# Kernel tuning notes

Measured on AMD Instinct MI355X. Metric: run time of the kernel, lower is better.

Reference implementation:

```python
import jax, jax.numpy as jnp
import numpy as np

WIN = 12          # max_relative_position
HEAD_DIM = 64     # E, equals num_units of relative-position tables


def _rel_embed(table, length):
    r = jnp.arange(length)
    idx = jnp.clip(r[None, :] - r[:, None], -WIN, WIN) + WIN  # [L, L]
    return table[idx]  # [L, L, E]


def setup_inputs() -> dict:
    key = jax.random.key(0)
    ks = jax.random.split(key, 7)
    B, L, H, E = 4, 1024, 8, HEAD_DIM
    shp = (B, L, H, E)
    xavier = float(np.sqrt(6.0 / (2 * WIN + 1 + E)))
    return {
        "x": jax.random.normal(ks[0], shp, jnp.float32),
        "y": jax.random.normal(ks[1], shp, jnp.float32),
        "v_x": jax.random.normal(ks[2], shp, jnp.float32),
        "v_y": jax.random.normal(ks[3], shp, jnp.float32),
        "rel_k_table": jax.random.uniform(ks[4], (2 * WIN + 1, E), jnp.float32, -xavier, xavier),
        "rel_vx_table": jax.random.uniform(ks[5], (2 * WIN + 1, E), jnp.float32, -xavier, xavier),
        "rel_vy_table": jax.random.uniform(ks[6], (2 * WIN + 1, E), jnp.float32, -xavier, xavier),
        "attn_mask1": jnp.zeros((1,), jnp.bool_),
        "attn_mask2": jnp.zeros((1,), jnp.bool_),
    }


def reference(x, y, v_x, v_y, rel_k_table, rel_vx_table, rel_vy_table, attn_mask1, attn_mask2):
    B, L, H, E = x.shape
    scale = 1.0 / float(np.sqrt(E))

    rel_k = _rel_embed(rel_k_table, L)    # [L, L, E]
    rel_vy = _rel_embed(rel_vy_table, L)  # [L, L, E]
    rel_vx = _rel_embed(rel_vx_table, L)  # [L, L, E]

    # scores1[b,h,l,s] = <x_bl h, y_bs h> + <x_bl h, rel_k[l,s]>
    scores1 = jnp.einsum('blhe,bshe->bhls', x, y) \
            + jnp.einsum('blhe,lse->bhls', x, rel_k)
    scores2 = jnp.swapaxes(scores1, -2, -1)  # pre-softmax transpose

    A1 = jax.nn.softmax(scale * scores1, axis=-1)  # [B,H,L,S]
    A2 = jax.nn.softmax(scale * scores2, axis=-1)

    V_Y = jnp.einsum('bhls,bshd->bhld', A1, v_y) \
        + jnp.einsum('bhls,lsd->bhld', A1, rel_vy)
    V_X = jnp.einsum('bhls,bshd->bhld', A2, v_x) \
        + jnp.einsum('bhls,lsd->bhld', A2, rel_vx)

    # module returns (V_Y^T, None, V_X^T, None); drop the Nones
    return jnp.swapaxes(V_Y, 1, 2), jnp.swapaxes(V_X, 1, 2)
```

## Files before the change

kernel.cpp:

```cpp
#include <hip/hip_runtime.h>
#include <math.h>

#define LQ 1024
#define RS 512
#define PJ 26
#define NP 32
#define ASCALE 0.18033688f

typedef __attribute__((ext_vector_type(4))) float f32x4;
typedef __attribute__((ext_vector_type(8))) short short8x;

__device__ __forceinline__ unsigned pk2(float a, float b) {
  unsigned r;
  asm("v_cvt_pk_bf16_f32 %0, %1, %2" : "=v"(r) : "v"(a), "v"(b));
  return r;
}

__device__ __forceinline__ int swz(int row, int bc) {
  return row * 128 + (bc ^ ((row & 7) << 4));
}
__device__ __forceinline__ int swzVT(int row, int bc) {
  return row * 128 + (bc ^ ((((row >> 3) ^ row) & 7) << 4));
}

__global__ __launch_bounds__(256) void k_relproj(const float* __restrict__ x,
                                                 const float* __restrict__ relk,
                                                 float* __restrict__ P) {
  __shared__ float rk[25][68];
  __shared__ float xs[64][68];
  const int tid = threadIdx.x;
  const int pair = blockIdx.y, l0 = blockIdx.x * 64;
  const int b = pair >> 3, h = pair & 7;
  for (int i = tid; i < 25 * 64; i += 256) rk[i >> 6][i & 63] = relk[i] * ASCALE;
  const int row = tid >> 2, q = tid & 3;
  const float* xr = x + (size_t)b * 524288 + (size_t)(l0 + row) * RS + h * 64 + q * 16;
#pragma unroll
  for (int i = 0; i < 4; ++i) {
    float4 a = *(const float4*)(xr + i * 4);
    xs[row][q * 16 + i * 4 + 0] = a.x; xs[row][q * 16 + i * 4 + 1] = a.y;
    xs[row][q * 16 + i * 4 + 2] = a.z; xs[row][q * 16 + i * 4 + 3] = a.w;
  }
  __syncthreads();
  float* Pr = P + ((size_t)pair * LQ + l0 + row) * PJ;
  for (int j = q; j < 25; j += 4) {
    float acc = 0.f;
#pragma unroll
    for (int e = 0; e < 64; ++e) acc += xs[row][e] * rk[j][e];
    Pr[j] = acc;
  }
}

__global__ __launch_bounds__(256, 2) void k_fused(
    const float* __restrict__ x, const float* __restrict__ y,
    const float* __restrict__ vx, const float* __restrict__ vy,
    const float* __restrict__ relvx, const float* __restrict__ relvy,
    const float* __restrict__ P_g, float* __restrict__ out_g) {
  __shared__ __align__(16) char U[8192];
  __shared__ __align__(16) char Bb[2][8192];
  __shared__ __align__(16) char Vb[2][8192];
  __shared__ float W[64 * PJ];

  const int tid = threadIdx.x;
  const int p = blockIdx.x;
  const int g = p & 63, bx = p >> 6;
  const int pair = g & 31, mode = g >> 5;
  const int b = pair >> 3, h = pair & 7;
  const int l0 = bx * 64;

  const float* Af = mode ? y : x;
  const float* Bl = mode ? x : y;
  const float* Vv = mode ? vx : vy;
  const float* tb = mode ? relvx : relvy;
  float* outp = out_g + (mode ? 2097152 : 0);

  const float* abase = Af + (size_t)b * 524288 + h * 64;
  const float* bbase = Bl + (size_t)b * 524288 + h * 64;
  const float* vbase = Vv + (size_t)b * 524288 + h * 64;
  const float* Pbase = P_g + (size_t)pair * LQ * PJ;
  float* outb = outp + (size_t)b * 524288 + h * 64;

  const int browA = tid >> 2, bqA = tid & 3;
  const int vsb = tid >> 4, vdb = tid & 15;

  {
    const float* s = abase + (size_t)(l0 + browA) * RS + bqA * 16;
#pragma unroll
    for (int hh = 0; hh < 2; ++hh) {
      float4 a = *(const float4*)(s + hh * 8);
      float4 c = *(const float4*)(s + hh * 8 + 4);
      uint4 u;
      u.x = pk2(a.x * ASCALE, a.y * ASCALE); u.y = pk2(a.z * ASCALE, a.w * ASCALE);
      u.z = pk2(c.x * ASCALE, c.y * ASCALE); u.w = pk2(c.z * ASCALE, c.w * ASCALE);
      *(uint4*)(U + swz(browA, bqA * 32 + hh * 16)) = u;
    }
    const float* sb2 = bbase + (size_t)browA * RS + bqA * 16;
#pragma unroll
    for (int hh = 0; hh < 2; ++hh) {
      float4 a = *(const float4*)(sb2 + hh * 8);
      float4 c = *(const float4*)(sb2 + hh * 8 + 4);
      uint4 u;
      u.x = pk2(a.x, a.y); u.y = pk2(a.z, a.w);
      u.z = pk2(c.x, c.y); u.w = pk2(c.z, c.w);
      *(uint4*)(Bb[0] + swz(browA, bqA * 32 + hh * 16)) = u;
    }
    const float* sv = vbase + (size_t)vsb * 4 * RS + vdb * 4;
    float4 r0 = *(const float4*)(sv);
    float4 r1 = *(const float4*)(sv + RS);
    float4 r2 = *(const float4*)(sv + 2 * RS);
    float4 r3 = *(const float4*)(sv + 3 * RS);
    uint2 w2;
    w2.x = pk2(r0.x, r1.x); w2.y = pk2(r2.x, r3.x);
    *(uint2*)(Vb[0] + swzVT(vdb * 4 + 0, vsb * 8)) = w2;
    w2.x = pk2(r0.y, r1.y); w2.y = pk2(r2.y, r3.y);
    *(uint2*)(Vb[0] + swzVT(vdb * 4 + 1, vsb * 8)) = w2;
    w2.x = pk2(r0.z, r1.z); w2.y = pk2(r2.z, r3.z);
    *(uint2*)(Vb[0] + swzVT(vdb * 4 + 2, vsb * 8)) = w2;
    w2.x = pk2(r0.w, r1.w); w2.y = pk2(r2.w, r3.w);
    *(uint2*)(Vb[0] + swzVT(vdb * 4 + 3, vsb * 8)) = w2;
  }
  for (int i = tid; i < 64 * PJ; i += 256) W[i] = 0.f;
  __syncthreads();

  const int lane = tid & 63, wv = tid >> 6;
  const int col16 = lane & 15, rg = lane >> 4;
  char* ea = U + wv * 2048;

  short8x af0 = *(const short8x*)(U + swz(wv * 16 + col16, rg * 16));
  short8x af1 = *(const short8x*)(U + swz(wv * 16 + col16, 64 + rg * 16));

  const int lloc = wv * 16 + col16;
  const float* ProwB = Pbase + (size_t)(l0 + lloc) * PJ;
  float bL = 0.f, bR = 0.f;
  if (mode == 0) { bL = ProwB[0]; bR = ProwB[24]; }

  f32x4 accO[4];
  float wl = 0.f, wr = 0.f;
  const f32x4 z4 = {0.f, 0.f, 0.f, 0.f};
#pragma unroll
  for (int dt = 0; dt < 4; ++dt) accO[dt] = z4;

  for (int t = 0; t < 16; ++t) {
    const int cb = t & 1, nb = cb ^ 1;
    const int rel0 = t * 64 - l0;
    const bool band = (rel0 >= -74 && rel0 <= 74);

    float4 pb[4], pv[4];
    if (t < 15) {
      const float* s = bbase + (size_t)((t + 1) * 64 + browA) * RS + bqA * 16;
#pragma unroll
      for (int i = 0; i < 4; ++i) pb[i] = *(const float4*)(s + i * 4);
      const float* sv2 = vbase + (size_t)((t + 1) * 64 + vsb * 4) * RS + vdb * 4;
#pragma unroll
      for (int k = 0; k < 4; ++k) pv[k] = *(const float4*)(sv2 + (size_t)k * RS);
    }

    float biasf[16];
    if (!band && mode == 1) {
      const bool right = rel0 > 0;
#pragma unroll
      for (int ct = 0; ct < 4; ++ct)
#pragma unroll
        for (int r = 0; r < 4; ++r)
          biasf[ct * 4 + r] =
              Pbase[(size_t)(t * 64 + ct * 16 + rg * 4 + r) * PJ + (right ? 0 : 24)];
    }

    f32x4 accS[4];
    const char* bB = Bb[cb];
#pragma unroll
    for (int ct = 0; ct < 4; ++ct) {
      short8x bf0 = *(const short8x*)(bB + swz(ct * 16 + col16, rg * 16));
      short8x bf1 = *(const short8x*)(bB + swz(ct * 16 + col16, 64 + rg * 16));
      f32x4 tacc = __builtin_amdgcn_mfma_f32_16x16x32_bf16(bf0, af0, z4, 0, 0, 0);
      accS[ct] = __builtin_amdgcn_mfma_f32_16x16x32_bf16(bf1, af1, tacc, 0, 0, 0);
    }

    if (!band) {
      const bool right = rel0 > 0;
      const float b0 = right ? bR : bL;
#pragma unroll
      for (int ct = 0; ct < 4; ++ct) {
        float e0 = __builtin_exp2f(accS[ct][0] + (mode ? biasf[ct * 4 + 0] : b0));
        float e1 = __builtin_exp2f(accS[ct][1] + (mode ? biasf[ct * 4 + 1] : b0));
        float e2 = __builtin_exp2f(accS[ct][2] + (mode ? biasf[ct * 4 + 2] : b0));
        float e3 = __builtin_exp2f(accS[ct][3] + (mode ? biasf[ct * 4 + 3] : b0));
        float s4 = (e0 + e1) + (e2 + e3);
        if (right) wr += s4; else wl += s4;
        uint2 w2; w2.x = pk2(e0, e1); w2.y = pk2(e2, e3);
        *(uint2*)(ea + swz(col16, ct * 32 + rg * 8)) = w2;
      }
    } else {
#pragma unroll
      for (int ct = 0; ct < 4; ++ct) {
        float e[4];
#pragma unroll
        for (int r = 0; r < 4; ++r) {
          const int sl = ct * 16 + rg * 4 + r;
          const int d = rel0 + sl - lloc;
          const int j = (d < -12 ? -12 : (d > 12 ? 12 : d)) + 12;
          const float bias = (mode == 0) ? ProwB[j]
                                         : Pbase[(size_t)(t * 64 + sl) * PJ + (24 - j)];
          e[r] = __builtin_exp2f(accS[ct][r] + bias);
          if (d <= -12) wl += e[r];
          else if (d >= 12) wr += e[r];
          else W[lloc * PJ + (d + 12)] = e[r];
        }
        uint2 w2; w2.x = pk2(e[0], e[1]); w2.y = pk2(e[2], e[3]);
        *(uint2*)(ea + swz(col16, ct * 32 + rg * 8)) = w2;
      }
    }

    __builtin_amdgcn_sched_barrier(0);
    asm volatile("s_waitcnt lgkmcnt(0)" ::: "memory");
    __builtin_amdgcn_sched_barrier(0);

    const char* vB = Vb[cb];
    short8x ef0 = *(const short8x*)(ea + swz(col16, rg * 16));
    short8x ef1 = *(const short8x*)(ea + swz(col16, 64 + rg * 16));
#pragma unroll
    for (int dt = 0; dt < 4; ++dt) {
      short8x v0 = *(const short8x*)(vB + swzVT(dt * 16 + col16, rg * 16));
      short8x v1 = *(const short8x*)(vB + swzVT(dt * 16 + col16, 64 + rg * 16));
      f32x4 tacc = __builtin_amdgcn_mfma_f32_16x16x32_bf16(ef0, v0, accO[dt], 0, 0, 0);
      accO[dt] = __builtin_amdgcn_mfma_f32_16x16x32_bf16(ef1, v1, tacc, 0, 0, 0);
    }

    if (t < 15) {
      uint4 u;
      u.x = pk2(pb[0].x, pb[0].y); u.y = pk2(pb[0].z, pb[0].w);
      u.z = pk2(pb[1].x, pb[1].y); u.w = pk2(pb[1].z, pb[1].w);
      *(uint4*)(Bb[nb] + swz(browA, bqA * 32)) = u;
      u.x = pk2(pb[2].x, pb[2].y); u.y = pk2(pb[2].z, pb[2].w);
      u.z = pk2(pb[3].x, pb[3].y); u.w = pk2(pb[3].z, pb[3].w);
      *(uint4*)(Bb[nb] + swz(browA, bqA * 32 + 16)) = u;
      uint2 w2;
      w2.x = pk2(pv[0].x, pv[1].x); w2.y = pk2(pv[2].x, pv[3].x);
      *(uint2*)(Vb[nb] + swzVT(vdb * 4 + 0, vsb * 8)) = w2;
      w2.x = pk2(pv[0].y, pv[1].y); w2.y = pk2(pv[2].y, pv[3].y);
      *(uint2*)(Vb[nb] + swzVT(vdb * 4 + 1, vsb * 8)) = w2;
      w2.x = pk2(pv[0].z, pv[1].z); w2.y = pk2(pv[2].z, pv[3].z);
      *(uint2*)(Vb[nb] + swzVT(vdb * 4 + 2, vsb * 8)) = w2;
      w2.x = pk2(pv[0].w, pv[1].w); w2.y = pk2(pv[2].w, pv[3].w);
      *(uint2*)(Vb[nb] + swzVT(vdb * 4 + 3, vsb * 8)) = w2;
    }
    __syncthreads();
  }

  float* tabf = (float*)U;
  for (int i = tid; i < 25 * 64; i += 256) tabf[i] = tb[i];
  __syncthreads();

  wl += __shfl_xor(wl, 16); wl += __shfl_xor(wl, 32);
  wr += __shfl_xor(wr, 16); wr += __shfl_xor(wr, 32);
  float wlR[4], wrR[4];
#pragma unroll
  for (int r = 0; r < 4; ++r) {
    const int src = rg * 4 + r;
    wlR[r] = __shfl(wl, src);
    wrR[r] = __shfl(wr, src);
  }

#pragma unroll
  for (int dt = 0; dt < 4; ++dt) {
    const int dd = dt * 16 + col16;
    const float t0 = tabf[dd], t24 = tabf[24 * 64 + dd];
#pragma unroll
    for (int r = 0; r < 4; ++r) accO[dt][r] += wlR[r] * t0 + wrR[r] * t24;
  }
  float wsum[4] = {0.f, 0.f, 0.f, 0.f};
#pragma unroll 4
  for (int j = 1; j < 24; ++j) {
    float tj[4];
#pragma unroll
    for (int dt = 0; dt < 4; ++dt) tj[dt] = tabf[j * 64 + dt * 16 + col16];
#pragma unroll
    for (int r = 0; r < 4; ++r) {
      const float w = W[(wv * 16 + rg * 4 + r) * PJ + j];
      wsum[r] += w;
#pragma unroll
      for (int dt = 0; dt < 4; ++dt) accO[dt][r] += w * tj[dt];
    }
  }
  float inv[4];
#pragma unroll
  for (int r = 0; r < 4; ++r) inv[r] = 1.f / (wlR[r] + wrR[r] + wsum[r]);

#pragma unroll
  for (int dt = 0; dt < 4; ++dt) {
#pragma unroll
    for (int r = 0; r < 4; ++r) {
      const int row = wv * 16 + rg * 4 + r;
      outb[(size_t)(l0 + row) * RS + dt * 16 + col16] = accO[dt][r] * inv[r];
    }
  }
}

extern "C" void kernel_launch(void* const* d_in, const int* in_sizes, int n_in,
                              void* d_out, int out_size, void* d_ws, size_t ws_size,
                              hipStream_t stream) {
  const float* x = (const float*)d_in[0];
  const float* y = (const float*)d_in[1];
  const float* vx = (const float*)d_in[2];
  const float* vy = (const float*)d_in[3];
  const float* relk = (const float*)d_in[4];
  const float* relvx = (const float*)d_in[5];
  const float* relvy = (const float*)d_in[6];
  float* out = (float*)d_out;

  float* P = (float*)d_ws;

  k_relproj<<<dim3(16, NP), 256, 0, stream>>>(x, relk, P);
  k_fused<<<dim3(1024), 256, 0, stream>>>(x, y, vx, vy, relvx, relvy, P, out);
}
```

Before: 90.91 us.

## Process two 64-row query tiles per block to reuse staged K/V tiles

Each block now covers 128 query rows, split into two 64-row halves, instead of 64, and the grid is halved to 512 blocks. Every staged bf16 B and V tile in shared memory feeds twice as many MFMAs, which halves global loads and conversion work for keys and values per query. The cost is doubled accumulator and score registers, larger shared memory for U and W, an extra barrier, and fewer blocks to spread across the GPU's compute units.

```diff
diff --git a/kernel.cpp b/kernel.cpp
--- a/kernel.cpp
+++ b/kernel.cpp
@@ -55,17 +55,17 @@
     const float* __restrict__ vx, const float* __restrict__ vy,
     const float* __restrict__ relvx, const float* __restrict__ relvy,
     const float* __restrict__ P_g, float* __restrict__ out_g) {
-  __shared__ __align__(16) char U[8192];
+  __shared__ __align__(16) char U[16384];
   __shared__ __align__(16) char Bb[2][8192];
   __shared__ __align__(16) char Vb[2][8192];
-  __shared__ float W[64 * PJ];
+  __shared__ float W[128 * PJ];
 
   const int tid = threadIdx.x;
   const int p = blockIdx.x;
   const int g = p & 63, bx = p >> 6;
   const int pair = g & 31, mode = g >> 5;
   const int b = pair >> 3, h = pair & 7;
-  const int l0 = bx * 64;
+  const int l0 = bx * 128;
 
   const float* Af = mode ? y : x;
   const float* Bl = mode ? x : y;
@@ -82,8 +82,9 @@
   const int browA = tid >> 2, bqA = tid & 3;
   const int vsb = tid >> 4, vdb = tid & 15;
 
-  {
-    const float* s = abase + (size_t)(l0 + browA) * RS + bqA * 16;
+#pragma unroll
+  for (int h2 = 0; h2 < 2; ++h2) {
+    const float* s = abase + (size_t)(l0 + h2 * 64 + browA) * RS + bqA * 16;
 #pragma unroll
     for (int hh = 0; hh < 2; ++hh) {
       float4 a = *(const float4*)(s + hh * 8);
@@ -91,8 +92,10 @@
       uint4 u;
       u.x = pk2(a.x * ASCALE, a.y * ASCALE); u.y = pk2(a.z * ASCALE, a.w * ASCALE);
       u.z = pk2(c.x * ASCALE, c.y * ASCALE); u.w = pk2(c.z * ASCALE, c.w * ASCALE);
-      *(uint4*)(U + swz(browA, bqA * 32 + hh * 16)) = u;
-    }
+      *(uint4*)(U + swz(h2 * 64 + browA, bqA * 32 + hh * 16)) = u;
+    }
+  }
+  {
     const float* sb2 = bbase + (size_t)browA * RS + bqA * 16;
 #pragma unroll
     for (int hh = 0; hh < 2; ++hh) {
@@ -118,31 +121,44 @@
     w2.x = pk2(r0.w, r1.w); w2.y = pk2(r2.w, r3.w);
     *(uint2*)(Vb[0] + swzVT(vdb * 4 + 3, vsb * 8)) = w2;
   }
-  for (int i = tid; i < 64 * PJ; i += 256) W[i] = 0.f;
+  for (int i = tid; i < 128 * PJ; i += 256) W[i] = 0.f;
   __syncthreads();
 
   const int lane = tid & 63, wv = tid >> 6;
   const int col16 = lane & 15, rg = lane >> 4;
-  char* ea = U + wv * 2048;
-
-  short8x af0 = *(const short8x*)(U + swz(wv * 16 + col16, rg * 16));
-  short8x af1 = *(const short8x*)(U + swz(wv * 16 + col16, 64 + rg * 16));
-
-  const int lloc = wv * 16 + col16;
-  const float* ProwB = Pbase + (size_t)(l0 + lloc) * PJ;
-  float bL = 0.f, bR = 0.f;
-  if (mode == 0) { bL = ProwB[0]; bR = ProwB[24]; }
-
-  f32x4 accO[4];
-  float wl = 0.f, wr = 0.f;
+
+  short8x af[2][2];
+#pragma unroll
+  for (int h2 = 0; h2 < 2; ++h2) {
+    af[h2][0] = *(const short8x*)(U + swz(h2 * 64 + wv * 16 + col16, rg * 16));
+    af[h2][1] = *(const short8x*)(U + swz(h2 * 64 + wv * 16 + col16, 64 + rg * 16));
+  }
+
+  const float* Prow[2];
+  float bL[2] = {0.f, 0.f}, bR[2] = {0.f, 0.f};
+#pragma unroll
+  for (int h2 = 0; h2 < 2; ++h2)
+    Prow[h2] = Pbase + (size_t)(l0 + h2 * 64 + wv * 16 + col16) * PJ;
+  if (mode == 0) {
+#pragma unroll
+    for (int h2 = 0; h2 < 2; ++h2) { bL[h2] = Prow[h2][0]; bR[h2] = Prow[h2][24]; }
+  }
+  __syncthreads();
+
+  f32x4 accO[2][4];
+  float wl[2] = {0.f, 0.f}, wr[2] = {0.f, 0.f};
   const f32x4 z4 = {0.f, 0.f, 0.f, 0.f};
 #pragma unroll
-  for (int dt = 0; dt < 4; ++dt) accO[dt] = z4;
+  for (int h2 = 0; h2 < 2; ++h2)
+#pragma unroll
+    for (int dt = 0; dt < 4; ++dt) accO[h2][dt] = z4;
 
   for (int t = 0; t < 16; ++t) {
     const int cb = t & 1, nb = cb ^ 1;
-    const int rel0 = t * 64 - l0;
-    const bool band = (rel0 >= -74 && rel0 <= 74);
+    const int relA = t * 64 - l0;
+    const int relB = relA - 64;
+    const bool fastA = (relA < -74 || relA > 74);
+    const bool fastB = (relB < -74 || relB > 74);
 
     float4 pb[4], pv[4];
     if (t < 15) {
@@ -155,8 +171,8 @@
     }
 
     float biasf[16];
-    if (!band && mode == 1) {
-      const bool right = rel0 > 0;
+    if (mode == 1 && (fastA || fastB)) {
+      const bool right = fastA ? (relA > 0) : (relB > 0);
 #pragma unroll
       for (int ct = 0; ct < 4; ++ct)
 #pragma unroll
@@ -165,48 +181,57 @@
               Pbase[(size_t)(t * 64 + ct * 16 + rg * 4 + r) * PJ + (right ? 0 : 24)];
     }
 
-    f32x4 accS[4];
+    f32x4 accS[2][4];
     const char* bB = Bb[cb];
 #pragma unroll
     for (int ct = 0; ct < 4; ++ct) {
       short8x bf0 = *(const short8x*)(bB + swz(ct * 16 + col16, rg * 16));
       short8x bf1 = *(const short8x*)(bB + swz(ct * 16 + col16, 64 + rg * 16));
-      f32x4 tacc = __builtin_amdgcn_mfma_f32_16x16x32_bf16(bf0, af0, z4, 0, 0, 0);
-      accS[ct] = __builtin_amdgcn_mfma_f32_16x16x32_bf16(bf1, af1, tacc, 0, 0, 0);
-    }
-
-    if (!band) {
-      const bool right = rel0 > 0;
-      const float b0 = right ? bR : bL;
-#pragma unroll
-      for (int ct = 0; ct < 4; ++ct) {
-        float e0 = __builtin_exp2f(accS[ct][0] + (mode ? biasf[ct * 4 + 0] : b0));
-        float e1 = __builtin_exp2f(accS[ct][1] + (mode ? biasf[ct * 4 + 1] : b0));
-        float e2 = __builtin_exp2f(accS[ct][2] + (mode ? biasf[ct * 4 + 2] : b0));
-        float e3 = __builtin_exp2f(accS[ct][3] + (mode ? biasf[ct * 4 + 3] : b0));
-        float s4 = (e0 + e1) + (e2 + e3);
-        if (right) wr += s4; else wl += s4;
-        uint2 w2; w2.x = pk2(e0, e1); w2.y = pk2(e2, e3);
-        *(uint2*)(ea + swz(col16, ct * 32 + rg * 8)) = w2;
-      }
-    } else {
-#pragma unroll
-      for (int ct = 0; ct < 4; ++ct) {
-        float e[4];
-#pragma unroll
-        for (int r = 0; r < 4; ++r) {
-          const int sl = ct * 16 + rg * 4 + r;
-          const int d = rel0 + sl - lloc;
-          const int j = (d < -12 ? -12 : (d > 12 ? 12 : d)) + 12;
-          const float bias = (mode == 0) ? ProwB[j]
-                                         : Pbase[(size_t)(t * 64 + sl) * PJ + (24 - j)];
-          e[r] = __builtin_exp2f(accS[ct][r] + bias);
-          if (d <= -12) wl += e[r];
-          else if (d >= 12) wr += e[r];
-          else W[lloc * PJ + (d + 12)] = e[r];
+      f32x4 t0 = __builtin_amdgcn_mfma_f32_16x16x32_bf16(bf0, af[0][0], z4, 0, 0, 0);
+      accS[0][ct] = __builtin_amdgcn_mfma_f32_16x16x32_bf16(bf1, af[0][1], t0, 0, 0, 0);
+      f32x4 t1 = __builtin_amdgcn_mfma_f32_16x16x32_bf16(bf0, af[1][0], z4, 0, 0, 0);
+      accS[1][ct] = __builtin_amdgcn_mfma_f32_16x16x32_bf16(bf1, af[1][1], t1, 0, 0, 0);
+    }
+
+#pragma unroll
+    for (int h2 = 0; h2 < 2; ++h2) {
+      const int rel = h2 ? relB : relA;
+      const bool fast = h2 ? fastB : fastA;
+      char* ea = U + (wv * 2 + h2) * 2048;
+      if (fast) {
+        const bool right = rel > 0;
+        const float b0 = right ? bR[h2] : bL[h2];
+#pragma unroll
+        for (int ct = 0; ct < 4; ++ct) {
+          float e0 = __builtin_exp2f(accS[h2][ct][0] + (mode ? biasf[ct * 4 + 0] : b0));
+          float e1 = __builtin_exp2f(accS[h2][ct][1] + (mode ? biasf[ct * 4 + 1] : b0));
+          float e2 = __builtin_exp2f(accS[h2][ct][2] + (mode ? biasf[ct * 4 + 2] : b0));
+          float e3 = __builtin_exp2f(accS[h2][ct][3] + (mode ? biasf[ct * 4 + 3] : b0));
+          float s4 = (e0 + e1) + (e2 + e3);
+          if (right) wr[h2] += s4; else wl[h2] += s4;
+          uint2 w2; w2.x = pk2(e0, e1); w2.y = pk2(e2, e3);
+          *(uint2*)(ea + swz(col16, ct * 32 + rg * 8)) = w2;
         }
-        uint2 w2; w2.x = pk2(e[0], e[1]); w2.y = pk2(e[2], e[3]);
-        *(uint2*)(ea + swz(col16, ct * 32 + rg * 8)) = w2;
+      } else {
+#pragma unroll
+        for (int ct = 0; ct < 4; ++ct) {
+          float e[4];
+#pragma unroll
+          for (int r = 0; r < 4; ++r) {
+            const int sl = ct * 16 + rg * 4 + r;
+            const int d = rel + sl - (wv * 16 + col16);
+            const int j = (d < -12 ? -12 : (d > 12 ? 12 : d)) + 12;
+            const float bias = (mode == 0)
+                ? Prow[h2][j]
+                : Pbase[(size_t)(t * 64 + sl) * PJ + (24 - j)];
+            e[r] = __builtin_exp2f(accS[h2][ct][r] + bias);
+            if (d <= -12) wl[h2] += e[r];
+            else if (d >= 12) wr[h2] += e[r];
+            else W[(h2 * 64 + wv * 16 + col16) * PJ + (d + 12)] = e[r];
+          }
+          uint2 w2; w2.x = pk2(e[0], e[1]); w2.y = pk2(e[2], e[3]);
+          *(uint2*)(ea + swz(col16, ct * 32 + rg * 8)) = w2;
+        }
       }
     }
 
@@ -215,14 +240,21 @@
     __builtin_amdgcn_sched_barrier(0);
 
     const char* vB = Vb[cb];
-    short8x ef0 = *(const short8x*)(ea + swz(col16, rg * 16));
-    short8x ef1 = *(const short8x*)(ea + swz(col16, 64 + rg * 16));
+    short8x ef[2][2];
+#pragma unroll
+    for (int h2 = 0; h2 < 2; ++h2) {
+      const char* ea = U + (wv * 2 + h2) * 2048;
+      ef[h2][0] = *(const short8x*)(ea + swz(col16, rg * 16));
+      ef[h2][1] = *(const short8x*)(ea + swz(col16, 64 + rg * 16));
+    }
 #pragma unroll
     for (int dt = 0; dt < 4; ++dt) {
       short8x v0 = *(const short8x*)(vB + swzVT(dt * 16 + col16, rg * 16));
       short8x v1 = *(const short8x*)(vB + swzVT(dt * 16 + col16, 64 + rg * 16));
-      f32x4 tacc = __builtin_amdgcn_mfma_f32_16x16x32_bf16(ef0, v0, accO[dt], 0, 0, 0);
-      accO[dt] = __builtin_amdgcn_mfma_f32_16x16x32_bf16(ef1, v1, tacc, 0, 0, 0);
+      f32x4 t0 = __builtin_amdgcn_mfma_f32_16x16x32_bf16(ef[0][0], v0, accO[0][dt], 0, 0, 0);
+      accO[0][dt] = __builtin_amdgcn_mfma_f32_16x16x32_bf16(ef[0][1], v1, t0, 0, 0, 0);
+      f32x4 t1 = __builtin_amdgcn_mfma_f32_16x16x32_bf16(ef[1][0], v0, accO[1][dt], 0, 0, 0);
+      accO[1][dt] = __builtin_amdgcn_mfma_f32_16x16x32_bf16(ef[1][1], v1, t1, 0, 0, 0);
     }
 
     if (t < 15) {
@@ -250,14 +282,17 @@
   for (int i = tid; i < 25 * 64; i += 256) tabf[i] = tb[i];
   __syncthreads();
 
-  wl += __shfl_xor(wl, 16); wl += __shfl_xor(wl, 32);
-  wr += __shfl_xor(wr, 16); wr += __shfl_xor(wr, 32);
-  float wlR[4], wrR[4];
-#pragma unroll
-  for (int r = 0; r < 4; ++r) {
-    const int src = rg * 4 + r;
-    wlR[r] = __shfl(wl, src);
-    wrR[r] = __shfl(wr, src);
+  float wlR[2][4], wrR[2][4];
+#pragma unroll
+  for (int h2 = 0; h2 < 2; ++h2) {
+    wl[h2] += __shfl_xor(wl[h2], 16); wl[h2] += __shfl_xor(wl[h2], 32);
+    wr[h2] += __shfl_xor(wr[h2], 16); wr[h2] += __shfl_xor(wr[h2], 32);
+#pragma unroll
+    for (int r = 0; r < 4; ++r) {
+      const int src = rg * 4 + r;
+      wlR[h2][r] = __shfl(wl[h2], src);
+      wrR[h2][r] = __shfl(wr[h2], src);
+    }
   }
 
 #pragma unroll
@@ -265,33 +300,40 @@
     const int dd = dt * 16 + col16;
     const float t0 = tabf[dd], t24 = tabf[24 * 64 + dd];
 #pragma unroll
-    for (int r = 0; r < 4; ++r) accO[dt][r] += wlR[r] * t0 + wrR[r] * t24;
-  }
-  float wsum[4] = {0.f, 0.f, 0.f, 0.f};
+    for (int h2 = 0; h2 < 2; ++h2)
+#pragma unroll
+      for (int r = 0; r < 4; ++r)
+        accO[h2][dt][r] += wlR[h2][r] * t0 + wrR[h2][r] * t24;
+  }
+  float wsum[2][4] = {{0.f, 0.f, 0.f, 0.f}, {0.f, 0.f, 0.f, 0.f}};
 #pragma unroll 4
   for (int j = 1; j < 24; ++j) {
     float tj[4];
 #pragma unroll
     for (int dt = 0; dt < 4; ++dt) tj[dt] = tabf[j * 64 + dt * 16 + col16];
 #pragma unroll
-    for (int r = 0; r < 4; ++r) {
-      const float w = W[(wv * 16 + rg * 4 + r) * PJ + j];
-      wsum[r] += w;
-#pragma unroll
-      for (int dt = 0; dt < 4; ++dt) accO[dt][r] += w * tj[dt];
-    }
-  }
-  float inv[4];
-#pragma unroll
-  for (int r = 0; r < 4; ++r) inv[r] = 1.f / (wlR[r] + wrR[r] + wsum[r]);
-
-#pragma unroll
-  for (int dt = 0; dt < 4; ++dt) {
-#pragma unroll
-    for (int r = 0; r < 4; ++r) {
-      const int row = wv * 16 + rg * 4 + r;
-      outb[(size_t)(l0 + row) * RS + dt * 16 + col16] = accO[dt][r] * inv[r];
-    }
+    for (int h2 = 0; h2 < 2; ++h2)
+#pragma unroll
+      for (int r = 0; r < 4; ++r) {
+        const float w = W[(h2 * 64 + wv * 16 + rg * 4 + r) * PJ + j];
+        wsum[h2][r] += w;
+#pragma unroll
+        for (int dt = 0; dt < 4; ++dt) accO[h2][dt][r] += w * tj[dt];
+      }
+  }
+#pragma unroll
+  for (int h2 = 0; h2 < 2; ++h2) {
+    float inv[4];
+#pragma unroll
+    for (int r = 0; r < 4; ++r)
+      inv[r] = 1.f / (wlR[h2][r] + wrR[h2][r] + wsum[h2][r]);
+#pragma unroll
+    for (int dt = 0; dt < 4; ++dt)
+#pragma unroll
+      for (int r = 0; r < 4; ++r) {
+        const int row = h2 * 64 + wv * 16 + rg * 4 + r;
+        outb[(size_t)(l0 + row) * RS + dt * 16 + col16] = accO[h2][dt][r] * inv[r];
+      }
   }
 }
 
@@ -310,5 +352,5 @@
   float* P = (float*)d_ws;
 
   k_relproj<<<dim3(16, NP), 256, 0, stream>>>(x, relk, P);
-  k_fused<<<dim3(1024), 256, 0, stream>>>(x, y, vx, vy, relvx, relvy, P, out);
-}
+  k_fused<<<dim3(512), 256, 0, stream>>>(x, y, vx, vy, relvx, relvy, P, out);
+}
```

Result: faster. 77.24 us, median of 2 (-15.0%).

## Double query tile to 128 rows with 512-thread blocks sharing K/V tiles

Applied to the files above, without the earlier changes.

Each block now covers 128 query rows using 8 waves, so every staged bf16 K and V tile in shared memory serves twice as many query rows. This halves global-to-LDS traffic and the conversion work per output. The band test becomes per-wave instead of per-block, so fewer waves fall onto the slow banded bias path. In exchange the grid halves to 512 blocks, LDS per block grows, and a larger block can lower occupancy and latency hiding.

```diff
diff --git a/kernel.cpp b/kernel.cpp
--- a/kernel.cpp
+++ b/kernel.cpp
@@ -50,22 +50,22 @@
   }
 }
 
-__global__ __launch_bounds__(256, 2) void k_fused(
+__global__ __launch_bounds__(512, 4) void k_fused(
     const float* __restrict__ x, const float* __restrict__ y,
     const float* __restrict__ vx, const float* __restrict__ vy,
     const float* __restrict__ relvx, const float* __restrict__ relvy,
     const float* __restrict__ P_g, float* __restrict__ out_g) {
-  __shared__ __align__(16) char U[8192];
+  __shared__ __align__(16) char U[16384];
   __shared__ __align__(16) char Bb[2][8192];
   __shared__ __align__(16) char Vb[2][8192];
-  __shared__ float W[64 * PJ];
+  __shared__ float W[128 * PJ];
 
   const int tid = threadIdx.x;
   const int p = blockIdx.x;
   const int g = p & 63, bx = p >> 6;
   const int pair = g & 31, mode = g >> 5;
   const int b = pair >> 3, h = pair & 7;
-  const int l0 = bx * 64;
+  const int l0 = bx * 128;
 
   const float* Af = mode ? y : x;
   const float* Bl = mode ? x : y;
@@ -79,11 +79,12 @@
   const float* Pbase = P_g + (size_t)pair * LQ * PJ;
   float* outb = outp + (size_t)b * 524288 + h * 64;
 
-  const int browA = tid >> 2, bqA = tid & 3;
-  const int vsb = tid >> 4, vdb = tid & 15;
+  const int rowA = tid >> 2, qA = tid & 3;
+  const int rowB = tid >> 3, qB = tid & 7;
+  const int vq = tid & 31, vs2 = tid >> 5;
 
   {
-    const float* s = abase + (size_t)(l0 + browA) * RS + bqA * 16;
+    const float* s = abase + (size_t)(l0 + rowA) * RS + qA * 16;
 #pragma unroll
     for (int hh = 0; hh < 2; ++hh) {
       float4 a = *(const float4*)(s + hh * 8);
@@ -91,34 +92,28 @@
       uint4 u;
       u.x = pk2(a.x * ASCALE, a.y * ASCALE); u.y = pk2(a.z * ASCALE, a.w * ASCALE);
       u.z = pk2(c.x * ASCALE, c.y * ASCALE); u.w = pk2(c.z * ASCALE, c.w * ASCALE);
-      *(uint4*)(U + swz(browA, bqA * 32 + hh * 16)) = u;
-    }
-    const float* sb2 = bbase + (size_t)browA * RS + bqA * 16;
-#pragma unroll
-    for (int hh = 0; hh < 2; ++hh) {
-      float4 a = *(const float4*)(sb2 + hh * 8);
-      float4 c = *(const float4*)(sb2 + hh * 8 + 4);
-      uint4 u;
-      u.x = pk2(a.x, a.y); u.y = pk2(a.z, a.w);
-      u.z = pk2(c.x, c.y); u.w = pk2(c.z, c.w);
-      *(uint4*)(Bb[0] + swz(browA, bqA * 32 + hh * 16)) = u;
-    }
-    const float* sv = vbase + (size_t)vsb * 4 * RS + vdb * 4;
-    float4 r0 = *(const float4*)(sv);
-    float4 r1 = *(const float4*)(sv + RS);
-    float4 r2 = *(const float4*)(sv + 2 * RS);
-    float4 r3 = *(const float4*)(sv + 3 * RS);
+      *(uint4*)(U + swz(rowA, qA * 32 + hh * 16)) = u;
+    }
+    const float* sb2 = bbase + (size_t)rowB * RS + qB * 8;
+    float4 a = *(const float4*)(sb2);
+    float4 c = *(const float4*)(sb2 + 4);
+    uint4 u;
+    u.x = pk2(a.x, a.y); u.y = pk2(a.z, a.w);
+    u.z = pk2(c.x, c.y); u.w = pk2(c.z, c.w);
+    *(uint4*)(Bb[0] + swz(rowB, qB * 16)) = u;
+
+    const float* sv = vbase + (size_t)(vs2 * 4) * RS + vq * 2;
+    float2 r0 = *(const float2*)(sv);
+    float2 r1 = *(const float2*)(sv + RS);
+    float2 r2 = *(const float2*)(sv + 2 * RS);
+    float2 r3 = *(const float2*)(sv + 3 * RS);
     uint2 w2;
     w2.x = pk2(r0.x, r1.x); w2.y = pk2(r2.x, r3.x);
-    *(uint2*)(Vb[0] + swzVT(vdb * 4 + 0, vsb * 8)) = w2;
+    *(uint2*)(Vb[0] + swzVT(vq * 2 + 0, vs2 * 8)) = w2;
     w2.x = pk2(r0.y, r1.y); w2.y = pk2(r2.y, r3.y);
-    *(uint2*)(Vb[0] + swzVT(vdb * 4 + 1, vsb * 8)) = w2;
-    w2.x = pk2(r0.z, r1.z); w2.y = pk2(r2.z, r3.z);
-    *(uint2*)(Vb[0] + swzVT(vdb * 4 + 2, vsb * 8)) = w2;
-    w2.x = pk2(r0.w, r1.w); w2.y = pk2(r2.w, r3.w);
-    *(uint2*)(Vb[0] + swzVT(vdb * 4 + 3, vsb * 8)) = w2;
-  }
-  for (int i = tid; i < 64 * PJ; i += 256) W[i] = 0.f;
+    *(uint2*)(Vb[0] + swzVT(vq * 2 + 1, vs2 * 8)) = w2;
+  }
+  for (int i = tid; i < 128 * PJ; i += 512) W[i] = 0.f;
   __syncthreads();
 
   const int lane = tid & 63, wv = tid >> 6;
@@ -132,6 +127,7 @@
   const float* ProwB = Pbase + (size_t)(l0 + lloc) * PJ;
   float bL = 0.f, bR = 0.f;
   if (mode == 0) { bL = ProwB[0]; bR = ProwB[24]; }
+  __syncthreads();
 
   f32x4 accO[4];
   float wl = 0.f, wr = 0.f;
@@ -141,22 +137,25 @@
 
   for (int t = 0; t < 16; ++t) {
     const int cb = t & 1, nb = cb ^ 1;
-    const int rel0 = t * 64 - l0;
-    const bool band = (rel0 >= -74 && rel0 <= 74);
-
-    float4 pb[4], pv[4];
+    const int rel = t * 64 - l0 - wv * 16;
+    const bool fast = (rel < -74 || rel > 26);
+
+    float4 pb0, pb1;
+    float2 pv0, pv1, pv2, pv3;
     if (t < 15) {
-      const float* s = bbase + (size_t)((t + 1) * 64 + browA) * RS + bqA * 16;
-#pragma unroll
-      for (int i = 0; i < 4; ++i) pb[i] = *(const float4*)(s + i * 4);
-      const float* sv2 = vbase + (size_t)((t + 1) * 64 + vsb * 4) * RS + vdb * 4;
-#pragma unroll
-      for (int k = 0; k < 4; ++k) pv[k] = *(const float4*)(sv2 + (size_t)k * RS);
+      const float* s = bbase + (size_t)((t + 1) * 64 + rowB) * RS + qB * 8;
+      pb0 = *(const float4*)(s);
+      pb1 = *(const float4*)(s + 4);
+      const float* sv2 = vbase + (size_t)((t + 1) * 64 + vs2 * 4) * RS + vq * 2;
+      pv0 = *(const float2*)(sv2);
+      pv1 = *(const float2*)(sv2 + RS);
+      pv2 = *(const float2*)(sv2 + 2 * RS);
+      pv3 = *(const float2*)(sv2 + 3 * RS);
     }
 
     float biasf[16];
-    if (!band && mode == 1) {
-      const bool right = rel0 > 0;
+    if (mode == 1 && fast) {
+      const bool right = rel > 0;
 #pragma unroll
       for (int ct = 0; ct < 4; ++ct)
 #pragma unroll
@@ -175,8 +174,8 @@
       accS[ct] = __builtin_amdgcn_mfma_f32_16x16x32_bf16(bf1, af1, tacc, 0, 0, 0);
     }
 
-    if (!band) {
-      const bool right = rel0 > 0;
+    if (fast) {
+      const bool right = rel > 0;
       const float b0 = right ? bR : bL;
 #pragma unroll
       for (int ct = 0; ct < 4; ++ct) {
@@ -196,7 +195,7 @@
 #pragma unroll
         for (int r = 0; r < 4; ++r) {
           const int sl = ct * 16 + rg * 4 + r;
-          const int d = rel0 + sl - lloc;
+          const int d = rel + sl - col16;
           const int j = (d < -12 ? -12 : (d > 12 ? 12 : d)) + 12;
           const float bias = (mode == 0) ? ProwB[j]
                                          : Pbase[(size_t)(t * 64 + sl) * PJ + (24 - j)];
@@ -227,27 +226,20 @@
 
     if (t < 15) {
       uint4 u;
-      u.x = pk2(pb[0].x, pb[0].y); u.y = pk2(pb[0].z, pb[0].w);
-      u.z = pk2(pb[1].x, pb[1].y); u.w = pk2(pb[1].z, pb[1].w);
-      *(uint4*)(Bb[nb] + swz(browA, bqA * 32)) = u;
-      u.x = pk2(pb[2].x, pb[2].y); u.y = pk2(pb[2].z, pb[2].w);
-      u.z = pk2(pb[3].x, pb[3].y); u.w = pk2(pb[3].z, pb[3].w);
-      *(uint4*)(Bb[nb] + swz(browA, bqA * 32 + 16)) = u;
+      u.x = pk2(pb0.x, pb0.y); u.y = pk2(pb0.z, pb0.w);
+      u.z = pk2(pb1.x, pb1.y); u.w = pk2(pb1.z, pb1.w);
+      *(uint4*)(Bb[nb] + swz(rowB, qB * 16)) = u;
       uint2 w2;
-      w2.x = pk2(pv[0].x, pv[1].x); w2.y = pk2(pv[2].x, pv[3].x);
-      *(uint2*)(Vb[nb] + swzVT(vdb * 4 + 0, vsb * 8)) = w2;
-      w2.x = pk2(pv[0].y, pv[1].y); w2.y = pk2(pv[2].y, pv[3].y);
-      *(uint2*)(Vb[nb] + swzVT(vdb * 4 + 1, vsb * 8)) = w2;
-      w2.x = pk2(pv[0].z, pv[1].z); w2.y = pk2(pv[2].z, pv[3].z);
-      *(uint2*)(Vb[nb] + swzVT(vdb * 4 + 2, vsb * 8)) = w2;
-      w2.x = pk2(pv[0].w, pv[1].w); w2.y = pk2(pv[2].w, pv[3].w);
-      *(uint2*)(Vb[nb] + swzVT(vdb * 4 + 3, vsb * 8)) = w2;
+      w2.x = pk2(pv0.x, pv1.x); w2.y = pk2(pv2.x, pv3.x);
+      *(uint2*)(Vb[nb] + swzVT(vq * 2 + 0, vs2 * 8)) = w2;
+      w2.x = pk2(pv0.y, pv1.y); w2.y = pk2(pv2.y, pv3.y);
+      *(uint2*)(Vb[nb] + swzVT(vq * 2 + 1, vs2 * 8)) = w2;
     }
     __syncthreads();
   }
 
   float* tabf = (float*)U;
-  for (int i = tid; i < 25 * 64; i += 256) tabf[i] = tb[i];
+  for (int i = tid; i < 25 * 64; i += 512) tabf[i] = tb[i];
   __syncthreads();
 
   wl += __shfl_xor(wl, 16); wl += __shfl_xor(wl, 32);
@@ -310,5 +302,5 @@
   float* P = (float*)d_ws;
 
   k_relproj<<<dim3(16, NP), 256, 0, stream>>>(x, relk, P);
-  k_fused<<<dim3(1024), 256, 0, stream>>>(x, y, vx, vy, relvx, relvy, P, out);
-}
+  k_fused<<<dim3(512), 512, 0, stream>>>(x, y, vx, vy, relvx, relvy, P, out);
+}
```

New measurement: 85.93 us. 1.06x faster.
